# Performance work log

Hardware: AMD Instinct MI355X
Metric: run time of the kernel (lower is better)

## Reference

```python
import jax, jax.numpy as jnp
import numpy as np
import math

B, S, E, H = 2, 2048, 1024, 16
D = E // H  # d_attn = 64
SCALE = 1.0 / math.sqrt(D)


def setup_inputs() -> dict:
    key = jax.random.key(0)
    ks = jax.random.split(key, 5)
    std = 0.02
    return {
        "q": jax.random.normal(ks[0], (B, S, E), dtype=jnp.float32),
        "Wq": jax.random.normal(ks[1], (E, H * D), dtype=jnp.float32) * std,
        "Wk": jax.random.normal(ks[2], (E, H * D), dtype=jnp.float32) * std,
        "Wv": jax.random.normal(ks[3], (E, H * D), dtype=jnp.float32) * std,
        "Wo": jax.random.normal(ks[4], (H * D, E), dtype=jnp.float32) * std,
        "gamma": jnp.ones((H,), dtype=jnp.float32),
    }


def reference(q, Wq, Wk, Wv, Wo, gamma):
    Bq, Sq, _ = q.shape
    # projections -> [B, H, S, D]
    qh = (q @ Wq).reshape(Bq, Sq, H, D).transpose(0, 2, 1, 3)
    kh = (q @ Wk).reshape(Bq, Sq, H, D).transpose(0, 2, 1, 3)
    vh = (q @ Wv).reshape(Bq, Sq, H, D).transpose(0, 2, 1, 3)
    # RBF distance scores: ||q||^2 - 2 q.k + ||k||^2, clamped at 0
    q_norm = jnp.sum(qh * qh, axis=-1, keepdims=True)          # [B,H,S,1]
    k_norm = jnp.sum(kh * kh, axis=-1, keepdims=True)          # [B,H,S,1]
    qk = jnp.einsum("bhsd,bhtd->bhst", qh, kh)                # [B,H,S,S]
    dist = jnp.maximum(q_norm - 2.0 * qk + jnp.swapaxes(k_norm, -2, -1), 0.0)
    scores = jnp.exp(-gamma[None, :, None, None] * SCALE * dist)
    # source: masked_fill(causal_mask == 0, 0) with mask = triu(ones, 1)
    # -> scores kept only on the STRICT upper triangle (faithful to source)
    mask = jnp.triu(jnp.ones((Sq, Sq), dtype=bool), k=1)
    scores = jnp.where(mask, scores, 0.0)
    out = jnp.einsum("bhst,bhtd->bhsd", scores, vh)            # [B,H,S,D]
    out = out.transpose(0, 2, 1, 3).reshape(Bq, Sq, H * D)
    return out @ Wo
```

## Files before the change

kernel.cpp:

```cpp
#include <hip/hip_runtime.h>
#include <stdint.h>

#define SCALE 0.125f
#define GSL_C 0.180336880111f

typedef short s16x8 __attribute__((ext_vector_type(8)));
typedef float f32x4 __attribute__((ext_vector_type(4)));

__device__ __forceinline__ unsigned short f2bf(float x){
  union { float f; unsigned int u; } v; v.f = x;
  unsigned int r = v.u + 0x7fffu + ((v.u >> 16) & 1u);
  return (unsigned short)(r >> 16);
}
__device__ __forceinline__ float bf2f(unsigned short u){
  union { unsigned int u; float f; } v; v.u = ((unsigned int)u) << 16;
  return v.f;
}
__device__ __forceinline__ f32x4 mfma16(s16x8 a, s16x8 b, f32x4 c){
  return __builtin_amdgcn_mfma_f32_16x16x32_bf16(a, b, c, 0, 0, 0);
}
__device__ __forceinline__ void gld_lds16(const void* g, void* l){
  __builtin_amdgcn_global_load_lds(
      (const __attribute__((address_space(1))) unsigned int*)g,
      (__attribute__((address_space(3))) unsigned int*)l, 16, 0, 0);
}
__device__ __forceinline__ unsigned int cvtpk(float lo, float hi){
  unsigned int r;
  asm("v_cvt_pk_bf16_f32 %0, %1, %2" : "=v"(r) : "v"(lo), "v"(hi));
  return r;
}

__global__ __launch_bounds__(256) void cast_kernel(const float* __restrict__ in,
                                                   unsigned short* __restrict__ out){
  int i = blockIdx.x*256 + threadIdx.x;
  const float4* p = (const float4*)in + (size_t)i*2;
  float4 a = p[0], b = p[1];
  unsigned short t[8] = {f2bf(a.x),f2bf(a.y),f2bf(a.z),f2bf(a.w),
                         f2bf(b.x),f2bf(b.y),f2bf(b.z),f2bf(b.w)};
  *(s16x8*)(out + (size_t)i*8) = *(const s16x8*)t;
}

__global__ __launch_bounds__(256) void wtrans_kernel(const float* __restrict__ W0,
    const float* __restrict__ W1, const float* __restrict__ W2, const float* __restrict__ W3,
    unsigned short* __restrict__ Wt){
  const float* src = (blockIdx.z==0)?W0:(blockIdx.z==1)?W1:(blockIdx.z==2)?W2:W3;
  unsigned short* dst = Wt + (size_t)blockIdx.z*1048576;
  int k0 = blockIdx.x*64, n0 = blockIdx.y*64;
  __shared__ unsigned short tile[64*72];
  int tid = threadIdx.x;
  int r = tid>>2, c = (tid&3)*16;
  const float* p = src + (size_t)(k0+r)*1024 + n0 + c;
  #pragma unroll
  for (int j=0;j<16;j++) tile[r*72 + c + j] = f2bf(p[j]);
  __syncthreads();
  int n = tid>>2, kc = (tid&3)*16;
  unsigned short o[16];
  #pragma unroll
  for (int j=0;j<16;j++) o[j] = tile[(kc+j)*72 + n];
  *(s16x8*)&dst[(size_t)(n0+n)*1024 + k0 + kc]     = *(const s16x8*)o;
  *(s16x8*)&dst[(size_t)(n0+n)*1024 + k0 + kc + 8] = *(const s16x8*)(o+8);
}

__global__ __launch_bounds__(256) void vtrans_kernel(const unsigned short* __restrict__ Vh,
    unsigned short* __restrict__ VtG){
  int bh = blockIdx.y, t0 = blockIdx.x*64;
  __shared__ unsigned short tile[64*72];
  int tid = threadIdx.x;
  #pragma unroll
  for (int p=0;p<2;p++){
    int idx = p*2048 + tid*8;
    int r = idx>>6, c = idx&63;
    *(s16x8*)&tile[r*72 + c] = *(const s16x8*)&Vh[((size_t)bh*2048 + t0 + r)*64 + c];
  }
  __syncthreads();
  #pragma unroll
  for (int p=0;p<2;p++){
    int idx = p*2048 + tid*8;
    int d = idx>>6, c = idx&63;
    unsigned short o[8];
    #pragma unroll
    for (int j=0;j<8;j++) o[j] = tile[(c+j)*72 + d];
    *(s16x8*)&VtG[((size_t)bh*64 + d)*2048 + t0 + c] = *(const s16x8*)o;
  }
}

template<int MODE>
__global__ __launch_bounds__(512) void gemm_db(const unsigned short* __restrict__ A,
    const unsigned short* __restrict__ Bt, unsigned short* __restrict__ outH,
    float* __restrict__ outF, float* __restrict__ qn, float* __restrict__ kn,
    const float* __restrict__ gamma){
  __shared__ short As[16384];
  __shared__ short Bs[16384];
  int tid = threadIdx.x;
  int w = tid>>6, l = tid&63;
  int lm = l & 15, hi = l >> 4;
  int wr = w>>1, wc = w&1;
  int m0 = blockIdx.x*128, n0 = blockIdx.y*128;

  const unsigned short* Bz;
  int bn0;
  if constexpr (MODE==1){ Bz = Bt + (size_t)(n0>>10)*1048576; bn0 = n0 & 1023; }
  else                  { Bz = Bt; bn0 = n0; }

  f32x4 acc[2][4];
  #pragma unroll
  for (int r=0;r<2;r++)
    #pragma unroll
    for (int c=0;c<4;c++){ f32x4 z = {0.f,0.f,0.f,0.f}; acc[r][c] = z; }

  int rsub = l>>3, csw = ((l&7) ^ (l>>3))*8;
  const unsigned short* gA = A  + (size_t)(m0  + w*16 + rsub)*1024 + csw;
  const unsigned short* gB = Bz + (size_t)(bn0 + w*16 + rsub)*1024 + csw;
  short* lA = As + w*1024;
  short* lB = Bs + w*1024;

  int ch0 = ((hi)     ^ (lm&7))*8;
  int ch1 = ((4 + hi) ^ (lm&7))*8;

  gld_lds16(gA,        lA);
  gld_lds16(gA + 8192, lA + 512);
  gld_lds16(gB,        lB);
  gld_lds16(gB + 8192, lB + 512);
  __syncthreads();

  const int NKT = 16;
  int buf = 0;
  for (int kt=0; kt<NKT; ++kt){
    if (kt+1 < NKT){
      const unsigned short* a = gA + (size_t)(kt+1)*64;
      const unsigned short* b = gB + (size_t)(kt+1)*64;
      short* dA = As + (buf^1)*8192 + w*1024;
      short* dB = Bs + (buf^1)*8192 + w*1024;
      gld_lds16(a,        dA);
      gld_lds16(a + 8192, dA + 512);
      gld_lds16(b,        dB);
      gld_lds16(b + 8192, dB + 512);
    }
    const short* curA = As + buf*8192;
    const short* curB = Bs + buf*8192;
    s16x8 af[2][2], bfv[4][2];
    #pragma unroll
    for (int r=0;r<2;r++){
      int ro = (wr*32 + r*16 + lm)*64;
      af[r][0] = *(const s16x8*)(curA + ro + ch0);
      af[r][1] = *(const s16x8*)(curA + ro + ch1);
    }
    #pragma unroll
    for (int c=0;c<4;c++){
      int ro = (wc*64 + c*16 + lm)*64;
      bfv[c][0] = *(const s16x8*)(curB + ro + ch0);
      bfv[c][1] = *(const s16x8*)(curB + ro + ch1);
    }
    __builtin_amdgcn_s_setprio(1);
    #pragma unroll
    for (int s=0;s<2;s++)
      #pragma unroll
      for (int r=0;r<2;r++)
        #pragma unroll
        for (int c=0;c<4;c++)
          acc[r][c] = mfma16(af[r][s], bfv[c][s], acc[r][c]);
    __builtin_amdgcn_s_setprio(0);
    __syncthreads();
    buf ^= 1;
  }

  if constexpr (MODE==0){
    #pragma unroll
    for (int r=0;r<2;r++)
      #pragma unroll
      for (int c=0;c<4;c++)
        #pragma unroll
        for (int i=0;i<4;i++){
          int m = m0 + wr*32 + r*16 + hi*4 + i;
          int n = n0 + wc*64 + c*16 + lm;
          outF[(size_t)m*1024 + n] = acc[r][c][i];
        }
  } else {
    int z = n0 >> 10;
    unsigned short* oz = outH + (size_t)z*4194304;
    #pragma unroll
    for (int r=0;r<2;r++){
      #pragma unroll
      for (int i=0;i<4;i++){
        int m = m0 + wr*32 + r*16 + hi*4 + i;
        int bq = m >> 11, sq = m & 2047;
        float nrm = 0.f;
        #pragma unroll
        for (int c=0;c<4;c++){
          int nn = (n0 & 1023) + wc*64 + c*16 + lm;
          int hq = nn >> 6, dq = nn & 63;
          int bh = bq*16 + hq;
          unsigned short bv = f2bf(acc[r][c][i]);
          oz[((size_t)bh*2048 + sq)*64 + dq] = bv;
          float vf = bf2f(bv);
          nrm = fmaf(vf, vf, nrm);
        }
        if (z < 2){
          nrm += __shfl_xor(nrm, 1);
          nrm += __shfl_xor(nrm, 2);
          nrm += __shfl_xor(nrm, 4);
          nrm += __shfl_xor(nrm, 8);
          if (lm == 0){
            int hq = ((n0 & 1023) + wc*64) >> 6;
            float gsl_h = gamma[hq] * GSL_C;
            float* dst = z ? kn : qn;
            dst[(size_t)(bq*16 + hq)*2048 + sq] = nrm * gsl_h;
          }
        }
      }
    }
  }
}

__global__ __launch_bounds__(256) void attn_kernel(const unsigned short* __restrict__ Qh,
    const unsigned short* __restrict__ Kh, const unsigned short* __restrict__ VtG,
    const float* __restrict__ qn, const float* __restrict__ kn,
    const float* __restrict__ gamma, unsigned short* __restrict__ attnO){
  __shared__ short Ks[2][4096];
  __shared__ short Vs[2][4096];
  __shared__ short Ps[4][1024];

  int bid = blockIdx.x;
  int bh = bid & 31; int b = bh>>4, h = bh&15;
  int rr = bid >> 5;
  int g = rr >> 3, r8 = rr & 7;
  int si = (g==0) ? r8 : (g==1) ? (31-r8) : (g==2) ? (8+r8) : (23-r8);
  int s0 = si*64;
  int tid = threadIdx.x, w = tid>>6, l = tid&63;
  int lm = l & 15, hi = l >> 4;
  float gs2l = 2.f * gamma[h] * GSL_C;

  int sq = s0 + w*16 + lm;
  const unsigned short* qbase = Qh + ((size_t)bh*2048 + sq)*64;
  s16x8 qf0 = *(const s16x8*)(qbase + hi*8);
  s16x8 qf1 = *(const s16x8*)(qbase + 32 + hi*8);
  float gq = -qn[(size_t)bh*2048 + sq];
  const float* knp = kn + (size_t)bh*2048;

  int chs = ((l&7) ^ (l>>3))*8;
  const unsigned short* kp0 = Kh  + ((size_t)bh*2048 + s0 + w*8 + (l>>3))*64 + chs;
  const unsigned short* vp0 = VtG + ((size_t)bh*64 + w*8 + (l>>3))*2048 + s0 + chs;

  f32x4 accO[4];
  #pragma unroll
  for (int df=0; df<4; df++){ f32x4 zz = {0.f,0.f,0.f,0.f}; accO[df] = zz; }

  gld_lds16(kp0,           &Ks[0][w*512]);
  gld_lds16(kp0 + 32*64,   &Ks[0][w*512 + 2048]);
  gld_lds16(vp0,           &Vs[0][w*512]);
  gld_lds16(vp0 + 32*2048, &Vs[0][w*512 + 2048]);
  __syncthreads();

  int swl = (lm & 7) << 4;
  int cur = 0;
  for (int t0 = s0; t0 < 2048; t0 += 64, cur ^= 1){
    int nxt = t0 + 64;
    if (nxt < 2048){
      int dt = nxt - s0;
      const unsigned short* kp = kp0 + (size_t)dt*64;
      const unsigned short* vp = vp0 + dt;
      gld_lds16(kp,           &Ks[cur^1][w*512]);
      gld_lds16(kp + 32*64,   &Ks[cur^1][w*512 + 2048]);
      gld_lds16(vp,           &Vs[cur^1][w*512]);
      gld_lds16(vp + 32*2048, &Vs[cur^1][w*512 + 2048]);
    }
    const char* kbase = (const char*)&Ks[cur][0];
    const char* vbase = (const char*)&Vs[cur][0];
    char* pbase = (char*)&Ps[w][0];

    #pragma unroll
    for (int tf=0; tf<4; tf++){
      int ro = (tf*16 + lm)*128;
      s16x8 ka = *(const s16x8*)(kbase + ro + ((hi*16) ^ swl));
      s16x8 kb = *(const s16x8*)(kbase + ro + ((64 + hi*16) ^ swl));
      f32x4 sc = {0.f,0.f,0.f,0.f};
      __builtin_amdgcn_s_setprio(1);
      sc = mfma16(ka, qf0, sc);
      sc = mfma16(kb, qf1, sc);
      __builtin_amdgcn_s_setprio(0);
      float4 knv = *(const float4*)(knp + t0 + tf*16 + hi*4);
      float a0 = fminf(fmaf(gs2l, sc[0], gq - knv.x), 0.f);
      float a1 = fminf(fmaf(gs2l, sc[1], gq - knv.y), 0.f);
      float a2 = fminf(fmaf(gs2l, sc[2], gq - knv.z), 0.f);
      float a3 = fminf(fmaf(gs2l, sc[3], gq - knv.w), 0.f);
      float e0 = __builtin_amdgcn_exp2f(a0);
      float e1 = __builtin_amdgcn_exp2f(a1);
      float e2 = __builtin_amdgcn_exp2f(a2);
      float e3 = __builtin_amdgcn_exp2f(a3);
      if (t0 == s0){
        int tbase = t0 + tf*16 + hi*4;
        e0 = (tbase + 0 > sq) ? e0 : 0.f;
        e1 = (tbase + 1 > sq) ? e1 : 0.f;
        e2 = (tbase + 2 > sq) ? e2 : 0.f;
        e3 = (tbase + 3 > sq) ? e3 : 0.f;
      }
      uint2 pk;
      pk.x = cvtpk(e0, e1);
      pk.y = cvtpk(e2, e3);
      int po = lm*128 + (((tf*32 + hi*8) ^ swl));
      *(uint2*)(pbase + po) = pk;
    }

    __builtin_amdgcn_s_setprio(1);
    #pragma unroll
    for (int kf=0; kf<2; kf++){
      s16x8 pa = *(const s16x8*)(pbase + lm*128 + ((kf*64 + hi*16) ^ swl));
      #pragma unroll
      for (int df=0; df<4; df++){
        int vo = (df*16 + lm)*128 + ((kf*64 + hi*16) ^ swl);
        s16x8 vb = *(const s16x8*)(vbase + vo);
        accO[df] = mfma16(pa, vb, accO[df]);
      }
    }
    __builtin_amdgcn_s_setprio(0);
    __syncthreads();
  }

  #pragma unroll
  for (int df=0; df<4; df++)
    #pragma unroll
    for (int i=0; i<4; i++){
      int s = s0 + w*16 + hi*4 + i;
      attnO[((size_t)b*2048 + s)*1024 + h*64 + df*16 + lm] = f2bf(accO[df][i]);
    }
}

extern "C" void kernel_launch(void* const* d_in, const int* in_sizes, int n_in,
                              void* d_out, int out_size, void* d_ws, size_t ws_size,
                              hipStream_t stream){
  const float* q  = (const float*)d_in[0];
  const float* Wq = (const float*)d_in[1];
  const float* Wk = (const float*)d_in[2];
  const float* Wv = (const float*)d_in[3];
  const float* Wo = (const float*)d_in[4];
  const float* gm = (const float*)d_in[5];
  float* out = (float*)d_out;

  unsigned short* qbf = (unsigned short*)d_ws;
  unsigned short* Wt  = qbf + 4194304;
  unsigned short* Qh  = Wt  + 4194304;
  unsigned short* Kh  = Qh  + 4194304;
  unsigned short* Vh  = Kh  + 4194304;
  unsigned short* Vt  = Vh  + 4194304;
  unsigned short* aO  = Vt  + 4194304;
  float* qn = (float*)(aO + 4194304);
  float* kn = qn + 65536;

  cast_kernel  <<<2048, 256, 0, stream>>>(q, qbf);
  wtrans_kernel<<<dim3(16,16,4), 256, 0, stream>>>(Wq, Wk, Wv, Wo, Wt);
  gemm_db<1>   <<<dim3(32,24), 512, 0, stream>>>(qbf, Wt, Qh, nullptr, qn, kn, gm);
  vtrans_kernel<<<dim3(32,32), 256, 0, stream>>>(Vh, Vt);
  attn_kernel  <<<dim3(1024), 256, 0, stream>>>(Qh, Kh, Vt, qn, kn, gm, aO);
  gemm_db<0>   <<<dim3(32,8), 512, 0, stream>>>(aO, Wt + 3*1048576, nullptr, out, nullptr, nullptr, nullptr);
}
```

Measured before the change: 114.1 us.

## Double query rows per attention block to reuse K/V tiles across two query fragments

Each attention block now handles 128 query rows instead of 64, and each wave processes two 16-row query fragments that share the same K and V LDS fragments. This halves K/V global loads and LDS reads per unit of work and halves the grid to 512 blocks. Waves whose query rows lie entirely past the first key tile skip that tile, and masking now covers two tiles. The cost is more registers for accumulators, a larger P buffer, and fewer blocks, which may reduce occupancy or leave load imbalance on the causal triangle.

```diff
diff --git a/kernel.cpp b/kernel.cpp
--- a/kernel.cpp
+++ b/kernel.cpp
@@ -218,32 +218,38 @@
     const float* __restrict__ gamma, unsigned short* __restrict__ attnO){
   __shared__ short Ks[2][4096];
   __shared__ short Vs[2][4096];
-  __shared__ short Ps[4][1024];
+  __shared__ short Ps[4][2048];
 
   int bid = blockIdx.x;
   int bh = bid & 31; int b = bh>>4, h = bh&15;
-  int rr = bid >> 5;
-  int g = rr >> 3, r8 = rr & 7;
-  int si = (g==0) ? r8 : (g==1) ? (31-r8) : (g==2) ? (8+r8) : (23-r8);
-  int s0 = si*64;
+  int pr = bid >> 5;
+  int r8 = pr & 7;
+  int si = (pr < 8) ? r8 : (15 - r8);
+  int s0 = si*128;
   int tid = threadIdx.x, w = tid>>6, l = tid&63;
   int lm = l & 15, hi = l >> 4;
   float gs2l = 2.f * gamma[h] * GSL_C;
 
-  int sq = s0 + w*16 + lm;
-  const unsigned short* qbase = Qh + ((size_t)bh*2048 + sq)*64;
-  s16x8 qf0 = *(const s16x8*)(qbase + hi*8);
-  s16x8 qf1 = *(const s16x8*)(qbase + 32 + hi*8);
-  float gq = -qn[(size_t)bh*2048 + sq];
+  int q0 = s0 + w*32 + lm;
+  const unsigned short* qbA = Qh + ((size_t)bh*2048 + q0)*64;
+  const unsigned short* qbB = qbA + 16*64;
+  s16x8 qfA0 = *(const s16x8*)(qbA + hi*8);
+  s16x8 qfA1 = *(const s16x8*)(qbA + 32 + hi*8);
+  s16x8 qfB0 = *(const s16x8*)(qbB + hi*8);
+  s16x8 qfB1 = *(const s16x8*)(qbB + 32 + hi*8);
+  float gqA = -qn[(size_t)bh*2048 + q0];
+  float gqB = -qn[(size_t)bh*2048 + q0 + 16];
   const float* knp = kn + (size_t)bh*2048;
 
   int chs = ((l&7) ^ (l>>3))*8;
   const unsigned short* kp0 = Kh  + ((size_t)bh*2048 + s0 + w*8 + (l>>3))*64 + chs;
   const unsigned short* vp0 = VtG + ((size_t)bh*64 + w*8 + (l>>3))*2048 + s0 + chs;
 
-  f32x4 accO[4];
-  #pragma unroll
-  for (int df=0; df<4; df++){ f32x4 zz = {0.f,0.f,0.f,0.f}; accO[df] = zz; }
+  f32x4 accO[2][4];
+  #pragma unroll
+  for (int qb=0; qb<2; qb++)
+    #pragma unroll
+    for (int df=0; df<4; df++){ f32x4 zz = {0.f,0.f,0.f,0.f}; accO[qb][df] = zz; }
 
   gld_lds16(kp0,           &Ks[0][w*512]);
   gld_lds16(kp0 + 32*64,   &Ks[0][w*512 + 2048]);
@@ -264,65 +270,84 @@
       gld_lds16(vp,           &Vs[cur^1][w*512]);
       gld_lds16(vp + 32*2048, &Vs[cur^1][w*512 + 2048]);
     }
-    const char* kbase = (const char*)&Ks[cur][0];
-    const char* vbase = (const char*)&Vs[cur][0];
-    char* pbase = (char*)&Ps[w][0];
-
-    #pragma unroll
-    for (int tf=0; tf<4; tf++){
-      int ro = (tf*16 + lm)*128;
-      s16x8 ka = *(const s16x8*)(kbase + ro + ((hi*16) ^ swl));
-      s16x8 kb = *(const s16x8*)(kbase + ro + ((64 + hi*16) ^ swl));
-      f32x4 sc = {0.f,0.f,0.f,0.f};
+    bool dead = (t0 == s0) && (w >= 2);
+    if (!dead){
+      const char* kbase = (const char*)&Ks[cur][0];
+      const char* vbase = (const char*)&Vs[cur][0];
+      char* pbase = (char*)&Ps[w][0];
+      bool domask = (t0 - s0) < 128;
+
+      #pragma unroll
+      for (int tf=0; tf<4; tf++){
+        int ro = (tf*16 + lm)*128;
+        s16x8 ka = *(const s16x8*)(kbase + ro + ((hi*16) ^ swl));
+        s16x8 kb = *(const s16x8*)(kbase + ro + ((64 + hi*16) ^ swl));
+        f32x4 scA = {0.f,0.f,0.f,0.f};
+        f32x4 scB = {0.f,0.f,0.f,0.f};
+        __builtin_amdgcn_s_setprio(1);
+        scA = mfma16(ka, qfA0, scA);
+        scA = mfma16(kb, qfA1, scA);
+        scB = mfma16(ka, qfB0, scB);
+        scB = mfma16(kb, qfB1, scB);
+        __builtin_amdgcn_s_setprio(0);
+        float4 knv = *(const float4*)(knp + t0 + tf*16 + hi*4);
+        float eA0 = __builtin_amdgcn_exp2f(fminf(fmaf(gs2l, scA[0], gqA - knv.x), 0.f));
+        float eA1 = __builtin_amdgcn_exp2f(fminf(fmaf(gs2l, scA[1], gqA - knv.y), 0.f));
+        float eA2 = __builtin_amdgcn_exp2f(fminf(fmaf(gs2l, scA[2], gqA - knv.z), 0.f));
+        float eA3 = __builtin_amdgcn_exp2f(fminf(fmaf(gs2l, scA[3], gqA - knv.w), 0.f));
+        float eB0 = __builtin_amdgcn_exp2f(fminf(fmaf(gs2l, scB[0], gqB - knv.x), 0.f));
+        float eB1 = __builtin_amdgcn_exp2f(fminf(fmaf(gs2l, scB[1], gqB - knv.y), 0.f));
+        float eB2 = __builtin_amdgcn_exp2f(fminf(fmaf(gs2l, scB[2], gqB - knv.z), 0.f));
+        float eB3 = __builtin_amdgcn_exp2f(fminf(fmaf(gs2l, scB[3], gqB - knv.w), 0.f));
+        if (domask){
+          int tb = t0 + tf*16 + hi*4;
+          eA0 = (tb + 0 > q0) ? eA0 : 0.f;
+          eA1 = (tb + 1 > q0) ? eA1 : 0.f;
+          eA2 = (tb + 2 > q0) ? eA2 : 0.f;
+          eA3 = (tb + 3 > q0) ? eA3 : 0.f;
+          int qB = q0 + 16;
+          eB0 = (tb + 0 > qB) ? eB0 : 0.f;
+          eB1 = (tb + 1 > qB) ? eB1 : 0.f;
+          eB2 = (tb + 2 > qB) ? eB2 : 0.f;
+          eB3 = (tb + 3 > qB) ? eB3 : 0.f;
+        }
+        uint2 pkA, pkB;
+        pkA.x = cvtpk(eA0, eA1);
+        pkA.y = cvtpk(eA2, eA3);
+        pkB.x = cvtpk(eB0, eB1);
+        pkB.y = cvtpk(eB2, eB3);
+        int poA = lm*128 + ((tf*32 + hi*8) ^ swl);
+        *(uint2*)(pbase + poA)          = pkA;
+        *(uint2*)(pbase + poA + 16*128) = pkB;
+      }
+
       __builtin_amdgcn_s_setprio(1);
-      sc = mfma16(ka, qf0, sc);
-      sc = mfma16(kb, qf1, sc);
+      #pragma unroll
+      for (int kf=0; kf<2; kf++){
+        s16x8 paA = *(const s16x8*)(pbase + lm*128        + ((kf*64 + hi*16) ^ swl));
+        s16x8 paB = *(const s16x8*)(pbase + (16+lm)*128   + ((kf*64 + hi*16) ^ swl));
+        #pragma unroll
+        for (int df=0; df<4; df++){
+          int vo = (df*16 + lm)*128 + ((kf*64 + hi*16) ^ swl);
+          s16x8 vb = *(const s16x8*)(vbase + vo);
+          accO[0][df] = mfma16(paA, vb, accO[0][df]);
+          accO[1][df] = mfma16(paB, vb, accO[1][df]);
+        }
+      }
       __builtin_amdgcn_s_setprio(0);
-      float4 knv = *(const float4*)(knp + t0 + tf*16 + hi*4);
-      float a0 = fminf(fmaf(gs2l, sc[0], gq - knv.x), 0.f);
-      float a1 = fminf(fmaf(gs2l, sc[1], gq - knv.y), 0.f);
-      float a2 = fminf(fmaf(gs2l, sc[2], gq - knv.z), 0.f);
-      float a3 = fminf(fmaf(gs2l, sc[3], gq - knv.w), 0.f);
-      float e0 = __builtin_amdgcn_exp2f(a0);
-      float e1 = __builtin_amdgcn_exp2f(a1);
-      float e2 = __builtin_amdgcn_exp2f(a2);
-      float e3 = __builtin_amdgcn_exp2f(a3);
-      if (t0 == s0){
-        int tbase = t0 + tf*16 + hi*4;
-        e0 = (tbase + 0 > sq) ? e0 : 0.f;
-        e1 = (tbase + 1 > sq) ? e1 : 0.f;
-        e2 = (tbase + 2 > sq) ? e2 : 0.f;
-        e3 = (tbase + 3 > sq) ? e3 : 0.f;
+    }
+    __syncthreads();
+  }
+
+  #pragma unroll
+  for (int qb=0; qb<2; qb++)
+    #pragma unroll
+    for (int df=0; df<4; df++)
+      #pragma unroll
+      for (int i=0; i<4; i++){
+        int s = s0 + w*32 + qb*16 + hi*4 + i;
+        attnO[((size_t)b*2048 + s)*1024 + h*64 + df*16 + lm] = f2bf(accO[qb][df][i]);
       }
-      uint2 pk;
-      pk.x = cvtpk(e0, e1);
-      pk.y = cvtpk(e2, e3);
-      int po = lm*128 + (((tf*32 + hi*8) ^ swl));
-      *(uint2*)(pbase + po) = pk;
-    }
-
-    __builtin_amdgcn_s_setprio(1);
-    #pragma unroll
-    for (int kf=0; kf<2; kf++){
-      s16x8 pa = *(const s16x8*)(pbase + lm*128 + ((kf*64 + hi*16) ^ swl));
-      #pragma unroll
-      for (int df=0; df<4; df++){
-        int vo = (df*16 + lm)*128 + ((kf*64 + hi*16) ^ swl);
-        s16x8 vb = *(const s16x8*)(vbase + vo);
-        accO[df] = mfma16(pa, vb, accO[df]);
-      }
-    }
-    __builtin_amdgcn_s_setprio(0);
-    __syncthreads();
-  }
-
-  #pragma unroll
-  for (int df=0; df<4; df++)
-    #pragma unroll
-    for (int i=0; i<4; i++){
-      int s = s0 + w*16 + hi*4 + i;
-      attnO[((size_t)b*2048 + s)*1024 + h*64 + df*16 + lm] = f2bf(accO[df][i]);
-    }
 }
 
 extern "C" void kernel_launch(void* const* d_in, const int* in_sizes, int n_in,
@@ -350,6 +375,6 @@
   wtrans_kernel<<<dim3(16,16,4), 256, 0, stream>>>(Wq, Wk, Wv, Wo, Wt);
   gemm_db<1>   <<<dim3(32,24), 512, 0, stream>>>(qbf, Wt, Qh, nullptr, qn, kn, gm);
   vtrans_kernel<<<dim3(32,32), 256, 0, stream>>>(Vh, Vt);
-  attn_kernel  <<<dim3(1024), 256, 0, stream>>>(Qh, Kh, Vt, qn, kn, gm, aO);
+  attn_kernel  <<<dim3(512), 256, 0, stream>>>(Qh, Kh, Vt, qn, kn, gm, aO);
   gemm_db<0>   <<<dim3(32,8), 512, 0, stream>>>(aO, Wt + 3*1048576, nullptr, out, nullptr, nullptr, nullptr);
 }
```

Result: slower. 122.1 us (+7.0%).

## Switch attention to 32x32 MFMA with register-resident P via permlane swap

Applied to the files above, without the earlier changes.

The attention kernel moves from 16x16x32 to 32x32x16 bf16 MFMA tiles, with 2 waves of 32 query rows each per block instead of 4 waves of 16. The score-to-P conversion now stays in registers, using v_permlane32_swap to reshape the accumulator layout into an A operand, so the P LDS round trip is gone. Key sub-tiles that fall entirely below the diagonal are skipped. Fewer threads per block (128, launch bounds with 2 blocks per SIMD hint) change occupancy and double per-wave LDS staging work, and the larger accumulators raise register pressure.

```diff
diff --git a/kernel.cpp b/kernel.cpp
--- a/kernel.cpp
+++ b/kernel.cpp
@@ -6,6 +6,7 @@
 
 typedef short s16x8 __attribute__((ext_vector_type(8)));
 typedef float f32x4 __attribute__((ext_vector_type(4)));
+typedef float f32x16 __attribute__((ext_vector_type(16)));
 
 __device__ __forceinline__ unsigned short f2bf(float x){
   union { float f; unsigned int u; } v; v.f = x;
@@ -19,6 +20,9 @@
 __device__ __forceinline__ f32x4 mfma16(s16x8 a, s16x8 b, f32x4 c){
   return __builtin_amdgcn_mfma_f32_16x16x32_bf16(a, b, c, 0, 0, 0);
 }
+__device__ __forceinline__ f32x16 mfma32(s16x8 a, s16x8 b, f32x16 c){
+  return __builtin_amdgcn_mfma_f32_32x32x16_bf16(a, b, c, 0, 0, 0);
+}
 __device__ __forceinline__ void gld_lds16(const void* g, void* l){
   __builtin_amdgcn_global_load_lds(
       (const __attribute__((address_space(1))) unsigned int*)g,
@@ -28,6 +32,9 @@
   unsigned int r;
   asm("v_cvt_pk_bf16_f32 %0, %1, %2" : "=v"(r) : "v"(lo), "v"(hi));
   return r;
+}
+__device__ __forceinline__ void plswap(unsigned int &a, unsigned int &b){
+  asm("v_permlane32_swap_b32 %0, %1" : "+v"(a), "+v"(b));
 }
 
 __global__ __launch_bounds__(256) void cast_kernel(const float* __restrict__ in,
@@ -212,13 +219,12 @@
   }
 }
 
-__global__ __launch_bounds__(256) void attn_kernel(const unsigned short* __restrict__ Qh,
+__global__ __launch_bounds__(128, 2) void attn_kernel(const unsigned short* __restrict__ Qh,
     const unsigned short* __restrict__ Kh, const unsigned short* __restrict__ VtG,
     const float* __restrict__ qn, const float* __restrict__ kn,
     const float* __restrict__ gamma, unsigned short* __restrict__ attnO){
   __shared__ short Ks[2][4096];
   __shared__ short Vs[2][4096];
-  __shared__ short Ps[4][1024];
 
   int bid = blockIdx.x;
   int bh = bid & 31; int b = bh>>4, h = bh&15;
@@ -227,102 +233,119 @@
   int si = (g==0) ? r8 : (g==1) ? (31-r8) : (g==2) ? (8+r8) : (23-r8);
   int s0 = si*64;
   int tid = threadIdx.x, w = tid>>6, l = tid&63;
-  int lm = l & 15, hi = l >> 4;
+  int l31 = l & 31, hi5 = l >> 5, l7 = l & 7;
   float gs2l = 2.f * gamma[h] * GSL_C;
 
-  int sq = s0 + w*16 + lm;
-  const unsigned short* qbase = Qh + ((size_t)bh*2048 + sq)*64;
-  s16x8 qf0 = *(const s16x8*)(qbase + hi*8);
-  s16x8 qf1 = *(const s16x8*)(qbase + 32 + hi*8);
-  float gq = -qn[(size_t)bh*2048 + sq];
+  int q0 = s0 + w*32;
+  int qrow = q0 + l31;
+  const unsigned short* qb = Qh + ((size_t)bh*2048 + qrow)*64;
+  s16x8 qf[4];
+  #pragma unroll
+  for (int c=0;c<4;c++) qf[c] = *(const s16x8*)(qb + c*16 + hi5*8);
+  float gq = -qn[(size_t)bh*2048 + qrow];
   const float* knp = kn + (size_t)bh*2048;
 
-  int chs = ((l&7) ^ (l>>3))*8;
-  const unsigned short* kp0 = Kh  + ((size_t)bh*2048 + s0 + w*8 + (l>>3))*64 + chs;
-  const unsigned short* vp0 = VtG + ((size_t)bh*64 + w*8 + (l>>3))*2048 + s0 + chs;
-
-  f32x4 accO[4];
-  #pragma unroll
-  for (int df=0; df<4; df++){ f32x4 zz = {0.f,0.f,0.f,0.f}; accO[df] = zz; }
-
-  gld_lds16(kp0,           &Ks[0][w*512]);
-  gld_lds16(kp0 + 32*64,   &Ks[0][w*512 + 2048]);
-  gld_lds16(vp0,           &Vs[0][w*512]);
-  gld_lds16(vp0 + 32*2048, &Vs[0][w*512 + 2048]);
+  int chs = (l7 ^ (l>>3))*8;
+  const unsigned short* kp0 = Kh  + ((size_t)bh*2048 + s0 + w*32 + (l>>3))*64 + chs;
+  const unsigned short* vp0 = VtG + ((size_t)bh*64 + w*32 + (l>>3))*2048 + s0 + chs;
+
+  f32x16 accO0, accO1;
+  #pragma unroll
+  for (int r=0;r<16;r++){ accO0[r] = 0.f; accO1[r] = 0.f; }
+
+#define STAGE(bufi, dt) { \
+    const unsigned short* kp = kp0 + (size_t)(dt)*64; \
+    const unsigned short* vp = vp0 + (dt); \
+    short* dK = &Ks[bufi][w*2048]; \
+    short* dV = &Vs[bufi][w*2048]; \
+    gld_lds16(kp,         dK); \
+    gld_lds16(kp +  512,  dK + 512); \
+    gld_lds16(kp + 1024,  dK + 1024); \
+    gld_lds16(kp + 1536,  dK + 1536); \
+    gld_lds16(vp,         dV); \
+    gld_lds16(vp + 16384, dV + 512); \
+    gld_lds16(vp + 32768, dV + 1024); \
+    gld_lds16(vp + 49152, dV + 1536); \
+  }
+
+  STAGE(0, 0);
   __syncthreads();
 
-  int swl = (lm & 7) << 4;
   int cur = 0;
   for (int t0 = s0; t0 < 2048; t0 += 64, cur ^= 1){
-    int nxt = t0 + 64;
-    if (nxt < 2048){
-      int dt = nxt - s0;
-      const unsigned short* kp = kp0 + (size_t)dt*64;
-      const unsigned short* vp = vp0 + dt;
-      gld_lds16(kp,           &Ks[cur^1][w*512]);
-      gld_lds16(kp + 32*64,   &Ks[cur^1][w*512 + 2048]);
-      gld_lds16(vp,           &Vs[cur^1][w*512]);
-      gld_lds16(vp + 32*2048, &Vs[cur^1][w*512 + 2048]);
-    }
-    const char* kbase = (const char*)&Ks[cur][0];
-    const char* vbase = (const char*)&Vs[cur][0];
-    char* pbase = (char*)&Ps[w][0];
-
-    #pragma unroll
-    for (int tf=0; tf<4; tf++){
-      int ro = (tf*16 + lm)*128;
-      s16x8 ka = *(const s16x8*)(kbase + ro + ((hi*16) ^ swl));
-      s16x8 kb = *(const s16x8*)(kbase + ro + ((64 + hi*16) ^ swl));
-      f32x4 sc = {0.f,0.f,0.f,0.f};
+    if (t0 + 64 < 2048) STAGE(cur^1, t0 + 64 - s0);
+    const short* kb = &Ks[cur][0];
+    const short* vb = &Vs[cur][0];
+
+    #pragma unroll
+    for (int tb=0; tb<2; tb++){
+      int tbase = t0 + tb*32 - s0;
+      if (tbase + 31 <= w*32) continue;
+      f32x16 sc;
+      #pragma unroll
+      for (int r=0;r<16;r++) sc[r] = 0.f;
       __builtin_amdgcn_s_setprio(1);
-      sc = mfma16(ka, qf0, sc);
-      sc = mfma16(kb, qf1, sc);
+      #pragma unroll
+      for (int c=0;c<4;c++){
+        s16x8 kf = *(const s16x8*)(kb + (tb*32 + l31)*64 + (((2*c + hi5) ^ l7)*8));
+        sc = mfma32(kf, qf[c], sc);
+      }
       __builtin_amdgcn_s_setprio(0);
-      float4 knv = *(const float4*)(knp + t0 + tf*16 + hi*4);
-      float a0 = fminf(fmaf(gs2l, sc[0], gq - knv.x), 0.f);
-      float a1 = fminf(fmaf(gs2l, sc[1], gq - knv.y), 0.f);
-      float a2 = fminf(fmaf(gs2l, sc[2], gq - knv.z), 0.f);
-      float a3 = fminf(fmaf(gs2l, sc[3], gq - knv.w), 0.f);
-      float e0 = __builtin_amdgcn_exp2f(a0);
-      float e1 = __builtin_amdgcn_exp2f(a1);
-      float e2 = __builtin_amdgcn_exp2f(a2);
-      float e3 = __builtin_amdgcn_exp2f(a3);
-      if (t0 == s0){
-        int tbase = t0 + tf*16 + hi*4;
-        e0 = (tbase + 0 > sq) ? e0 : 0.f;
-        e1 = (tbase + 1 > sq) ? e1 : 0.f;
-        e2 = (tbase + 2 > sq) ? e2 : 0.f;
-        e3 = (tbase + 3 > sq) ? e3 : 0.f;
-      }
-      uint2 pk;
-      pk.x = cvtpk(e0, e1);
-      pk.y = cvtpk(e2, e3);
-      int po = lm*128 + (((tf*32 + hi*8) ^ swl));
-      *(uint2*)(pbase + po) = pk;
-    }
-
-    __builtin_amdgcn_s_setprio(1);
-    #pragma unroll
-    for (int kf=0; kf<2; kf++){
-      s16x8 pa = *(const s16x8*)(pbase + lm*128 + ((kf*64 + hi*16) ^ swl));
-      #pragma unroll
-      for (int df=0; df<4; df++){
-        int vo = (df*16 + lm)*128 + ((kf*64 + hi*16) ^ swl);
-        s16x8 vb = *(const s16x8*)(vbase + vo);
-        accO[df] = mfma16(pa, vb, accO[df]);
-      }
-    }
-    __builtin_amdgcn_s_setprio(0);
+      float e[16];
+      #pragma unroll
+      for (int gg=0; gg<4; gg++){
+        float4 knv = *(const float4*)(knp + t0 + tb*32 + gg*8 + hi5*4);
+        float ks4[4] = {knv.x, knv.y, knv.z, knv.w};
+        #pragma unroll
+        for (int i=0;i<4;i++){
+          int r = gg*4 + i;
+          e[r] = __builtin_amdgcn_exp2f(fminf(fmaf(gs2l, sc[r], gq - ks4[i]), 0.f));
+        }
+      }
+      if (tbase < w*32 + 32){
+        #pragma unroll
+        for (int r=0;r<16;r++){
+          int t = t0 + tb*32 + (r&3) + 8*(r>>2) + 4*hi5;
+          e[r] = (t > qrow) ? e[r] : 0.f;
+        }
+      }
+      unsigned int u0 = cvtpk(e[0],  e[1]),  u1 = cvtpk(e[2],  e[3]);
+      unsigned int u2 = cvtpk(e[4],  e[5]),  u3 = cvtpk(e[6],  e[7]);
+      unsigned int u4 = cvtpk(e[8],  e[9]),  u5 = cvtpk(e[10], e[11]);
+      unsigned int u6 = cvtpk(e[12], e[13]), u7 = cvtpk(e[14], e[15]);
+      plswap(u0, u2);
+      plswap(u1, u3);
+      plswap(u4, u6);
+      plswap(u5, u7);
+      unsigned int f0[4] = {u0, u1, u2, u3};
+      unsigned int f1[4] = {u4, u5, u6, u7};
+      s16x8 pa0 = *(const s16x8*)f0;
+      s16x8 pa1 = *(const s16x8*)f1;
+      __builtin_amdgcn_s_setprio(1);
+      {
+        int cg0 = 2*tb, cg1 = 2*tb + 1;
+        s16x8 v00 = *(const s16x8*)(vb + (l31)*64      + (((2*cg0 + hi5) ^ l7)*8));
+        s16x8 v01 = *(const s16x8*)(vb + (l31)*64      + (((2*cg1 + hi5) ^ l7)*8));
+        s16x8 v10 = *(const s16x8*)(vb + (32 + l31)*64 + (((2*cg0 + hi5) ^ l7)*8));
+        s16x8 v11 = *(const s16x8*)(vb + (32 + l31)*64 + (((2*cg1 + hi5) ^ l7)*8));
+        accO0 = mfma32(pa0, v00, accO0);
+        accO0 = mfma32(pa1, v01, accO0);
+        accO1 = mfma32(pa0, v10, accO1);
+        accO1 = mfma32(pa1, v11, accO1);
+      }
+      __builtin_amdgcn_s_setprio(0);
+    }
     __syncthreads();
   }
-
-  #pragma unroll
-  for (int df=0; df<4; df++)
-    #pragma unroll
-    for (int i=0; i<4; i++){
-      int s = s0 + w*16 + hi*4 + i;
-      attnO[((size_t)b*2048 + s)*1024 + h*64 + df*16 + lm] = f2bf(accO[df][i]);
-    }
+#undef STAGE
+
+  #pragma unroll
+  for (int r=0;r<16;r++){
+    int s = q0 + (r&3) + 8*(r>>2) + 4*hi5;
+    size_t base = ((size_t)b*2048 + s)*1024 + h*64;
+    attnO[base + l31]      = f2bf(accO0[r]);
+    attnO[base + 32 + l31] = f2bf(accO1[r]);
+  }
 }
 
 extern "C" void kernel_launch(void* const* d_in, const int* in_sizes, int n_in,
@@ -350,6 +373,6 @@
   wtrans_kernel<<<dim3(16,16,4), 256, 0, stream>>>(Wq, Wk, Wv, Wo, Wt);
   gemm_db<1>   <<<dim3(32,24), 512, 0, stream>>>(qbf, Wt, Qh, nullptr, qn, kn, gm);
   vtrans_kernel<<<dim3(32,32), 256, 0, stream>>>(Vh, Vt);
-  attn_kernel  <<<dim3(1024), 256, 0, stream>>>(Qh, Kh, Vt, qn, kn, gm, aO);
+  attn_kernel  <<<dim3(1024), 128, 0, stream>>>(Qh, Kh, Vt, qn, kn, gm, aO);
   gemm_db<0>   <<<dim3(32,8), 512, 0, stream>>>(aO, Wt + 3*1048576, nullptr, out, nullptr, nullptr, nullptr);
 }
```

Measured after the change: 117.6 us. +3.0%, slower.
